# Kernel tuning notes

Hardware: AMD Instinct MI355X
Metric: run time of the kernel (lower is better)

## Reference

```python
import jax, jax.numpy as jnp
import numpy as np

N = 100000
IN_CH = 256
HID = 64
OUT_CH = 40
E1 = 1_600_000
E2 = 3_200_000


def spmm(rows, cols, vals, x, n):
    # out[r] = sum over edges e with rows[e]==r of vals[e] * x[cols[e]]
    return jax.ops.segment_sum(vals[:, None] * x[cols], rows, num_segments=n)


def setup_inputs() -> dict:
    key = jax.random.key(0)
    ks = jax.random.split(key, 12)
    x = jax.random.normal(ks[0], (N, IN_CH), dtype=jnp.float32)
    edge_index = jax.random.randint(ks[1], (2, E1), 0, N, dtype=jnp.int32)
    adj_src = jax.random.randint(ks[2], (E1,), 0, N, dtype=jnp.int32)
    adj_dst = jax.random.randint(ks[3], (E1,), 0, N, dtype=jnp.int32)
    adj_val = jax.random.uniform(ks[4], (E1,), dtype=jnp.float32)
    adj2_src = jax.random.randint(ks[5], (E2,), 0, N, dtype=jnp.int32)
    adj2_dst = jax.random.randint(ks[6], (E2,), 0, N, dtype=jnp.int32)
    adj2_val = jax.random.uniform(ks[7], (E2,), dtype=jnp.float32)
    fc1_w = jax.random.normal(ks[8], (HID, IN_CH), dtype=jnp.float32) * (1.0 / np.sqrt(IN_CH))
    fc_out_w = jax.random.normal(ks[9], (OUT_CH, 3 * HID), dtype=jnp.float32) * (1.0 / np.sqrt(3 * HID))
    fc_out_b = jax.random.normal(ks[10], (OUT_CH,), dtype=jnp.float32) * 0.01
    return {"x": x, "edge_index": edge_index,
            "adj_src": adj_src, "adj_dst": adj_dst, "adj_val": adj_val,
            "adj2_src": adj2_src, "adj2_dst": adj2_dst, "adj2_val": adj2_val,
            "fc1_w": fc1_w, "fc_out_w": fc_out_w, "fc_out_b": fc_out_b}


def reference(x, edge_index, adj_src, adj_dst, adj_val,
              adj2_src, adj2_dst, adj2_val, fc1_w, fc_out_w, fc_out_b):
    # h0 = fc1(x), no bias
    h0 = x @ fc1_w.T                                  # [N, HID]
    # num_layers = 1: one round of 1-hop and 2-hop propagation
    h1 = spmm(adj_src, adj_dst, adj_val, h0, N)       # [N, HID]
    h2 = spmm(adj2_src, adj2_dst, adj2_val, h0, N)    # [N, HID]
    h = jnp.concatenate([h0, h1, h2], axis=1)         # [N, 3*HID]
    # dropout is identity in eval mode
    return h @ fc_out_w.T + fc_out_b                  # [N, OUT_CH]
```

## Files before the change

kernel.cpp:

```cpp
#include <hip/hip_runtime.h>

#define Nn 100000
#define INC 256
#define OC 40
#define GEL 5242880u
#define NB 1563
#define CAP64 3744
#define CHUNK 4096
#define OVFCAP 65536
#define BSTRIDE 264

#define MP_OFF   0
#define G_OFF    131072
#define GCUR_OFF (G_OFF + 20971520)
#define OVFC_OFF (GCUR_OFF + 6256)
#define OVFL_OFF (OVFC_OFF + 8)
#define PAY_OFF  (OVFL_OFF + OVFCAP*12)

typedef __attribute__((ext_vector_type(8))) short bf16x8;
typedef __attribute__((ext_vector_type(4))) float f32x4;

__device__ __forceinline__ unsigned short f2bf(float f) {
    unsigned b = __float_as_uint(f);
    b += 0x7FFFu + ((b >> 16) & 1u);
    return (unsigned short)(b >> 16);
}
__device__ __forceinline__ float bf2f(unsigned short u) {
    return __uint_as_float(((unsigned)u) << 16);
}

__device__ __forceinline__ void fma8(float4& a0, float4& a1, uint4 u, float v) {
    a0.x = fmaf(v, __uint_as_float(u.x << 16), a0.x);
    a0.y = fmaf(v, __uint_as_float(u.x & 0xFFFF0000u), a0.y);
    a0.z = fmaf(v, __uint_as_float(u.y << 16), a0.z);
    a0.w = fmaf(v, __uint_as_float(u.y & 0xFFFF0000u), a0.w);
    a1.x = fmaf(v, __uint_as_float(u.z << 16), a1.x);
    a1.y = fmaf(v, __uint_as_float(u.z & 0xFFFF0000u), a1.y);
    a1.z = fmaf(v, __uint_as_float(u.w << 16), a1.z);
    a1.w = fmaf(v, __uint_as_float(u.w & 0xFFFF0000u), a1.w);
}

__global__ void make_M(const float* __restrict__ fc1_w,
                       const float* __restrict__ fc_out_w,
                       unsigned short* __restrict__ Mb) {
    int j = blockIdx.x;
    int k = threadIdx.x;
    float acc = 0.f;
    if (j < 120) {
        int i = j / 40, o = j - i * 40;
        const float* wrow = fc_out_w + o * 192 + i * 64;
#pragma unroll 8
        for (int t = 0; t < 64; ++t)
            acc = fmaf(wrow[t], fc1_w[t * 256 + k], acc);
    }
    Mb[j * 256 + k] = (j < 120) ? f2bf(acc) : (unsigned short)0;
}

__global__ __launch_bounds__(512, 4) void gemm_mfma(
    const float* __restrict__ x, const unsigned short* __restrict__ Mb,
    const float* __restrict__ bias, float* __restrict__ out,
    unsigned short* __restrict__ g) {
    __shared__ unsigned short mlds[120 * BSTRIDE];
    const int tid = threadIdx.x;
    const int w = tid >> 6;
    const int l = tid & 63;
    const int lane15 = l & 15;
    const int quad = l >> 4;

    for (int i = tid; i < 3840; i += 512) {
        int r = i >> 5;
        int k8 = (i & 31) * 8;
        uint4 v = *(const uint4*)(Mb + r * 256 + k8);
        *(uint4*)(mlds + r * BSTRIDE + k8) = v;
    }
    __syncthreads();

    const int arow = blockIdx.x * 128 + w * 16 + lane15;
    const bool rok = arow < Nn;
    const float* xp = x + (size_t)arow * INC + quad * 8;

    f32x4 acc[8];
#pragma unroll
    for (int c = 0; c < 8; ++c) acc[c] = (f32x4){0.f, 0.f, 0.f, 0.f};

    float4 pa[3], pb_[3];
#pragma unroll
    for (int p = 0; p < 2; ++p) {
        pa[p] = make_float4(0, 0, 0, 0); pb_[p] = make_float4(0, 0, 0, 0);
        if (rok) { pa[p] = *(const float4*)(xp + p * 32); pb_[p] = *(const float4*)(xp + p * 32 + 4); }
    }

#pragma unroll
    for (int kt = 0; kt < 8; ++kt) {
        const int nb = (kt + 2) % 3;
        if (kt + 2 < 8) {
            pa[nb] = make_float4(0, 0, 0, 0); pb_[nb] = make_float4(0, 0, 0, 0);
            if (rok) {
                pa[nb] = *(const float4*)(xp + (kt + 2) * 32);
                pb_[nb] = *(const float4*)(xp + (kt + 2) * 32 + 4);
            }
        }
        const int cu = kt % 3;
        bf16x8 af;
        af[0] = (short)f2bf(pa[cu].x); af[1] = (short)f2bf(pa[cu].y);
        af[2] = (short)f2bf(pa[cu].z); af[3] = (short)f2bf(pa[cu].w);
        af[4] = (short)f2bf(pb_[cu].x); af[5] = (short)f2bf(pb_[cu].y);
        af[6] = (short)f2bf(pb_[cu].z); af[7] = (short)f2bf(pb_[cu].w);
        const unsigned short* bbase = mlds + kt * 32 + quad * 8 + lane15 * BSTRIDE;
#pragma unroll
        for (int ct = 0; ct < 8; ++ct) {
            if (ct * 16 >= 120) break;
            bf16x8 bf = *(const bf16x8*)(bbase + ct * 16 * BSTRIDE);
            acc[ct] = __builtin_amdgcn_mfma_f32_16x16x32_bf16(af, bf, acc[ct], 0, 0, 0);
        }
    }

#pragma unroll
    for (int ct = 0; ct < 8; ++ct) {
        int col = ct * 16 + lane15;
        if (col >= 120) continue;
        int ib = col / 40;
        int cc = col - ib * 40;
        float badd = (ib == 0) ? bias[cc] : 0.f;
#pragma unroll
        for (int reg = 0; reg < 4; ++reg) {
            int gr = blockIdx.x * 128 + w * 16 + quad * 4 + reg;
            if (gr >= Nn) continue;
            float v = acc[ct][reg] + badd;
            if (ib == 0) out[gr * 40 + cc] = v;
            else g[(unsigned)(ib - 1) * GEL + (unsigned)gr * 40u + cc] = f2bf(v);
        }
    }
}

__global__ __launch_bounds__(1024, 8) void partition(
    const int* __restrict__ s1, const int* __restrict__ d1, const float* __restrict__ v1, int E1,
    const int* __restrict__ s2, const int* __restrict__ d2, const float* __restrict__ v2, int E2,
    int* __restrict__ gcur, uint2* __restrict__ payload,
    int* __restrict__ ovf_cnt, unsigned* __restrict__ ovf) {
    __shared__ int cnt[NB];
    __shared__ int loff[NB + 1];
    __shared__ int gbase[NB];
    __shared__ int scanbuf[1024];
    __shared__ uint2 pay[CHUNK];
    __shared__ unsigned short dest16[CHUNK];

    const int t = threadIdx.x;
    const int Etot = E1 + E2;
    const int e0 = blockIdx.x * CHUNK;

    for (int i = t; i < NB; i += 1024) cnt[i] = 0;
    __syncthreads();

    int my_b[4]; int my_rank[4]; unsigned my_p[4]; float my_v[4]; bool my_ok[4];
#pragma unroll
    for (int j = 0; j < 4; ++j) {
        int e = e0 + j * 1024 + t;
        my_ok[j] = (e < Etot);
        if (my_ok[j]) {
            int s, d; float v; unsigned gbit;
            if (e < E1) { s = s1[e]; d = d1[e]; v = v1[e]; gbit = 0u; }
            else { int e2 = e - E1; s = s2[e2]; d = d2[e2]; v = v2[e2]; gbit = 1u; }
            my_b[j] = s >> 6;
            my_p[j] = (unsigned)d | (gbit << 17) | (((unsigned)s & 63u) << 18);
            my_v[j] = v;
            my_rank[j] = atomicAdd(&cnt[my_b[j]], 1);
        }
    }
    __syncthreads();

    int c0 = (2 * t < NB) ? cnt[2 * t] : 0;
    int c1 = (2 * t + 1 < NB) ? cnt[2 * t + 1] : 0;
    scanbuf[t] = c0 + c1;
    __syncthreads();
    for (int off = 1; off < 1024; off <<= 1) {
        int v = (t >= off) ? scanbuf[t - off] : 0;
        __syncthreads();
        scanbuf[t] += v;
        __syncthreads();
    }
    int ex = scanbuf[t] - (c0 + c1);
    if (2 * t < NB)     loff[2 * t] = ex;
    if (2 * t + 1 < NB) loff[2 * t + 1] = ex + c0;
    if (t == 1023)      loff[NB] = scanbuf[1023];
    __syncthreads();

    for (int i = t; i < NB; i += 1024) {
        int cc = cnt[i];
        gbase[i] = cc ? atomicAdd(&gcur[i], cc) : 0;
    }
    __syncthreads();

#pragma unroll
    for (int j = 0; j < 4; ++j) {
        if (my_ok[j]) {
            int lp = loff[my_b[j]] + my_rank[j];
            pay[lp] = make_uint2(my_p[j], __float_as_uint(my_v[j]));
            dest16[lp] = (unsigned short)my_b[j];
        }
    }
    __syncthreads();

    int tot = loff[NB];
    for (int i = t; i < tot; i += 1024) {
        int b = dest16[i];
        int go = gbase[b] + (i - loff[b]);
        if (go < CAP64) payload[(size_t)b * CAP64 + go] = pay[i];
        else {
            int op = atomicAdd(ovf_cnt, 1);
            if (op < OVFCAP) {
                unsigned px = pay[i].x;
                ovf[3 * op] = ((unsigned)b << 6) | ((px >> 18) & 63u);
                ovf[3 * op + 1] = px;
                ovf[3 * op + 2] = pay[i].y;
            }
        }
    }
}

__global__ __launch_bounds__(640, 7) void bucket_gather(
    const int* __restrict__ gcur, const uint2* __restrict__ payload,
    const unsigned short* __restrict__ g, float* __restrict__ out) {
    __shared__ unsigned spay[CAP64];
    __shared__ int cnt[64];
    __shared__ int sb[64];
    __shared__ int rs[65];
    __shared__ float4 red4[64][10];

    const int t = threadIdx.x;
    const int b = blockIdx.x;
    int n = gcur[b];
    n = (n < CAP64) ? n : CAP64;

    if (t < 64) cnt[t] = 0;
    __syncthreads();

    const uint2* pb = payload + (size_t)b * CAP64;

    uint2 pe[6]; int rk[6];
#pragma unroll
    for (int j = 0; j < 6; ++j) {
        int i = t + j * 640;
        if (i < n) {
            uint2 p = pb[i];
            pe[j] = p;
            rk[j] = atomicAdd(&cnt[(p.x >> 18) & 63u], 1);
        }
    }
    __syncthreads();

    if (t < 64) sb[t] = cnt[t];
    __syncthreads();
    for (int off = 1; off < 64; off <<= 1) {
        int v = 0;
        if (t < 64 && t >= off) v = sb[t - off];
        __syncthreads();
        if (t < 64) sb[t] += v;
        __syncthreads();
    }
    if (t < 64) rs[t] = sb[t] - cnt[t];
    if (t == 63) rs[64] = sb[63];
    __syncthreads();

#pragma unroll
    for (int j = 0; j < 6; ++j) {
        int i = t + j * 640;
        if (i < n) {
            uint2 p = pe[j];
            int pos = rs[(p.x >> 18) & 63u] + rk[j];
            unsigned q = (unsigned)(__uint_as_float(p.y) * 16383.f + 0.5f);
            spay[pos] = (p.x & 0x3FFFFu) | (q << 18);
        }
    }
    __syncthreads();

    const int le = t / 10;
    const int sub = t - le * 10;
    const int grp = (sub >= 5) ? 1 : 0;
    const int q8 = (sub - grp * 5) * 8;
    const float VS = 1.0f / 16383.0f;

    float4 a0 = make_float4(0.f, 0.f, 0.f, 0.f);
    float4 a1 = a0, b0 = a0, b1 = a0;
    const int estart = rs[le];
    const int eend = rs[le + 1];
    int e = estart + grp;
    for (; e + 6 < eend; e += 8) {
        unsigned p0 = spay[e], p1 = spay[e + 2], p2 = spay[e + 4], p3 = spay[e + 6];
        uint4 u0 = *(const uint4*)(g + (p0 & 0x3FFFFu) * 40u + q8);
        uint4 u1 = *(const uint4*)(g + (p1 & 0x3FFFFu) * 40u + q8);
        uint4 u2 = *(const uint4*)(g + (p2 & 0x3FFFFu) * 40u + q8);
        uint4 u3 = *(const uint4*)(g + (p3 & 0x3FFFFu) * 40u + q8);
        fma8(a0, a1, u0, (float)(p0 >> 18) * VS);
        fma8(b0, b1, u1, (float)(p1 >> 18) * VS);
        fma8(a0, a1, u2, (float)(p2 >> 18) * VS);
        fma8(b0, b1, u3, (float)(p3 >> 18) * VS);
    }
    for (; e < eend; e += 2) {
        unsigned p = spay[e];
        uint4 u = *(const uint4*)(g + (p & 0x3FFFFu) * 40u + q8);
        fma8(a0, a1, u, (float)(p >> 18) * VS);
    }
    a0.x += b0.x; a0.y += b0.y; a0.z += b0.z; a0.w += b0.w;
    a1.x += b1.x; a1.y += b1.y; a1.z += b1.z; a1.w += b1.w;

    const int c2 = (q8 >> 2);
    __syncthreads();
    if (grp == 1) { red4[le][c2] = a0; red4[le][c2 + 1] = a1; }
    __syncthreads();
    if (grp == 0) {
        float4 r0 = red4[le][c2];
        float4 r1 = red4[le][c2 + 1];
        int gr = b * 64 + le;
        if (gr < Nn && eend > estart) {
            float* po = out + gr * 40 + q8;
            float4 o0 = *(const float4*)po;
            o0.x += a0.x + r0.x; o0.y += a0.y + r0.y;
            o0.z += a0.z + r0.z; o0.w += a0.w + r0.w;
            *(float4*)po = o0;
            float4 o1 = *(const float4*)(po + 4);
            o1.x += a1.x + r1.x; o1.y += a1.y + r1.y;
            o1.z += a1.z + r1.z; o1.w += a1.w + r1.w;
            *(float4*)(po + 4) = o1;
        }
    }
}

__global__ __launch_bounds__(256) void ovf_scatter(
    const int* __restrict__ ovf_cnt, const unsigned* __restrict__ ovf,
    const unsigned short* __restrict__ g, float* __restrict__ out) {
    int n = *ovf_cnt;
    n = (n < OVFCAP) ? n : OVFCAP;
    int total = n * 40;
    for (int i = blockIdx.x * 256 + threadIdx.x; i < total; i += 2048) {
        int idx = i / 40, c = i % 40;
        unsigned s = ovf[3 * idx];
        unsigned p = ovf[3 * idx + 1];
        float v = __uint_as_float(ovf[3 * idx + 2]);
        unsigned rid = p & 0x3FFFFu;
        float gf = bf2f(g[rid * 40u + c]);
        unsafeAtomicAdd(out + s * 40 + c, v * gf);
    }
}

extern "C" void kernel_launch(void* const* d_in, const int* in_sizes, int n_in,
                              void* d_out, int out_size, void* d_ws, size_t ws_size,
                              hipStream_t stream) {
    const float* x        = (const float*)d_in[0];
    const int*   adj_src  = (const int*)d_in[2];
    const int*   adj_dst  = (const int*)d_in[3];
    const float* adj_val  = (const float*)d_in[4];
    const int*   adj2_src = (const int*)d_in[5];
    const int*   adj2_dst = (const int*)d_in[6];
    const float* adj2_val = (const float*)d_in[7];
    const float* fc1_w    = (const float*)d_in[8];
    const float* fc_out_w = (const float*)d_in[9];
    const float* fc_out_b = (const float*)d_in[10];
    float* out = (float*)d_out;

    char* ws = (char*)d_ws;
    unsigned short* Mb      = (unsigned short*)(ws + MP_OFF);
    unsigned short* g       = (unsigned short*)(ws + G_OFF);
    int*            gcur    = (int*)(ws + GCUR_OFF);
    int*            ovf_cnt = (int*)(ws + OVFC_OFF);
    unsigned*       ovf     = (unsigned*)(ws + OVFL_OFF);
    uint2*          payload = (uint2*)(ws + PAY_OFF);

    const int E1 = in_sizes[2];
    const int E2 = in_sizes[5];
    const int Etot = E1 + E2;

    make_M<<<128, 256, 0, stream>>>(fc1_w, fc_out_w, Mb);
    gemm_mfma<<<(Nn + 127) / 128, 512, 0, stream>>>(x, Mb, fc_out_b, out, g);

    hipMemsetAsync(gcur, 0, (OVFC_OFF - GCUR_OFF) + 8, stream);
    partition<<<(Etot + CHUNK - 1) / CHUNK, 1024, 0, stream>>>(
        adj_src, adj_dst, adj_val, E1, adj2_src, adj2_dst, adj2_val, E2,
        gcur, payload, ovf_cnt, ovf);
    bucket_gather<<<NB, 640, 0, stream>>>(gcur, payload, g, out);
    ovf_scatter<<<8, 256, 0, stream>>>(ovf_cnt, ovf, g, out);
}
```

Before: 384.5 us.

## Replace bucketed partition with per-row fixed-capacity edge slots via global atomics

```diff
diff --git a/kernel.cpp b/kernel.cpp
--- a/kernel.cpp
+++ b/kernel.cpp
@@ -4,17 +4,19 @@
 #define INC 256
 #define OC 40
 #define GEL 5242880u
-#define NB 1563
-#define CAP64 3744
-#define CHUNK 4096
+#define CAPR 96
+#define SPITCH 100
+#define NROWB 128
+#define GBLK 782
+#define NROWA (GBLK * NROWB)
 #define OVFCAP 65536
 #define BSTRIDE 264
 
 #define MP_OFF   0
 #define G_OFF    131072
 #define GCUR_OFF (G_OFF + 20971520)
-#define OVFC_OFF (GCUR_OFF + 6256)
-#define OVFL_OFF (OVFC_OFF + 8)
+#define OVFC_OFF (GCUR_OFF + 400384)
+#define OVFL_OFF (OVFC_OFF + 16)
 #define PAY_OFF  (OVFL_OFF + OVFCAP*12)
 
 typedef __attribute__((ext_vector_type(8))) short bf16x8;
@@ -133,160 +135,71 @@
     }
 }
 
-__global__ __launch_bounds__(1024, 8) void partition(
+__global__ __launch_bounds__(256, 8) void partition(
     const int* __restrict__ s1, const int* __restrict__ d1, const float* __restrict__ v1, int E1,
     const int* __restrict__ s2, const int* __restrict__ d2, const float* __restrict__ v2, int E2,
-    int* __restrict__ gcur, uint2* __restrict__ payload,
+    int* __restrict__ gcur, unsigned* __restrict__ payload,
     int* __restrict__ ovf_cnt, unsigned* __restrict__ ovf) {
-    __shared__ int cnt[NB];
-    __shared__ int loff[NB + 1];
-    __shared__ int gbase[NB];
-    __shared__ int scanbuf[1024];
-    __shared__ uint2 pay[CHUNK];
-    __shared__ unsigned short dest16[CHUNK];
-
     const int t = threadIdx.x;
     const int Etot = E1 + E2;
-    const int e0 = blockIdx.x * CHUNK;
-
-    for (int i = t; i < NB; i += 1024) cnt[i] = 0;
-    __syncthreads();
-
-    int my_b[4]; int my_rank[4]; unsigned my_p[4]; float my_v[4]; bool my_ok[4];
+    const int e0 = blockIdx.x * 1024;
 #pragma unroll
     for (int j = 0; j < 4; ++j) {
-        int e = e0 + j * 1024 + t;
-        my_ok[j] = (e < Etot);
-        if (my_ok[j]) {
-            int s, d; float v; unsigned gbit;
-            if (e < E1) { s = s1[e]; d = d1[e]; v = v1[e]; gbit = 0u; }
-            else { int e2 = e - E1; s = s2[e2]; d = d2[e2]; v = v2[e2]; gbit = 1u; }
-            my_b[j] = s >> 6;
-            my_p[j] = (unsigned)d | (gbit << 17) | (((unsigned)s & 63u) << 18);
-            my_v[j] = v;
-            my_rank[j] = atomicAdd(&cnt[my_b[j]], 1);
-        }
-    }
-    __syncthreads();
-
-    int c0 = (2 * t < NB) ? cnt[2 * t] : 0;
-    int c1 = (2 * t + 1 < NB) ? cnt[2 * t + 1] : 0;
-    scanbuf[t] = c0 + c1;
-    __syncthreads();
-    for (int off = 1; off < 1024; off <<= 1) {
-        int v = (t >= off) ? scanbuf[t - off] : 0;
-        __syncthreads();
-        scanbuf[t] += v;
-        __syncthreads();
-    }
-    int ex = scanbuf[t] - (c0 + c1);
-    if (2 * t < NB)     loff[2 * t] = ex;
-    if (2 * t + 1 < NB) loff[2 * t + 1] = ex + c0;
-    if (t == 1023)      loff[NB] = scanbuf[1023];
-    __syncthreads();
-
-    for (int i = t; i < NB; i += 1024) {
-        int cc = cnt[i];
-        gbase[i] = cc ? atomicAdd(&gcur[i], cc) : 0;
-    }
-    __syncthreads();
-
-#pragma unroll
-    for (int j = 0; j < 4; ++j) {
-        if (my_ok[j]) {
-            int lp = loff[my_b[j]] + my_rank[j];
-            pay[lp] = make_uint2(my_p[j], __float_as_uint(my_v[j]));
-            dest16[lp] = (unsigned short)my_b[j];
-        }
-    }
-    __syncthreads();
-
-    int tot = loff[NB];
-    for (int i = t; i < tot; i += 1024) {
-        int b = dest16[i];
-        int go = gbase[b] + (i - loff[b]);
-        if (go < CAP64) payload[(size_t)b * CAP64 + go] = pay[i];
+        int e = e0 + j * 256 + t;
+        if (e >= Etot) continue;
+        int s, d; float v; unsigned ghi;
+        if (e < E1) { s = s1[e]; d = d1[e]; v = v1[e]; ghi = 0u; }
+        else { int e2 = e - E1; s = s2[e2]; d = d2[e2]; v = v2[e2]; ghi = 1u << 17; }
+        unsigned q = (unsigned)(v * 16383.f + 0.5f);
+        unsigned p = (unsigned)d | ghi | (q << 18);
+        int pos = atomicAdd(&gcur[s], 1);
+        if (pos < CAPR) payload[(size_t)s * CAPR + pos] = p;
         else {
             int op = atomicAdd(ovf_cnt, 1);
             if (op < OVFCAP) {
-                unsigned px = pay[i].x;
-                ovf[3 * op] = ((unsigned)b << 6) | ((px >> 18) & 63u);
-                ovf[3 * op + 1] = px;
-                ovf[3 * op + 2] = pay[i].y;
+                ovf[3 * op] = (unsigned)s;
+                ovf[3 * op + 1] = p & 0x3FFFFu;
+                ovf[3 * op + 2] = __float_as_uint(v);
             }
         }
     }
 }
 
 __global__ __launch_bounds__(640, 7) void bucket_gather(
-    const int* __restrict__ gcur, const uint2* __restrict__ payload,
+    const int* __restrict__ gcur, const unsigned* __restrict__ payload,
     const unsigned short* __restrict__ g, float* __restrict__ out) {
-    __shared__ unsigned spay[CAP64];
-    __shared__ int cnt[64];
-    __shared__ int sb[64];
-    __shared__ int rs[65];
-    __shared__ float4 red4[64][10];
+    __shared__ unsigned spay[NROWB * SPITCH];
+    __shared__ int cnt[NROWB];
 
     const int t = threadIdx.x;
     const int b = blockIdx.x;
-    int n = gcur[b];
-    n = (n < CAP64) ? n : CAP64;
-
-    if (t < 64) cnt[t] = 0;
+
+    if (t < NROWB) {
+        int n = gcur[b * NROWB + t];
+        cnt[t] = (n < CAPR) ? n : CAPR;
+    }
+
+    const unsigned* pbase = payload + (size_t)b * (NROWB * CAPR);
+    for (int i = t; i < NROWB * CAPR / 4; i += 640) {
+        int row = i / (CAPR / 4);
+        int c4 = (i - row * (CAPR / 4)) * 4;
+        uint4 v = *(const uint4*)(pbase + row * CAPR + c4);
+        *(uint4*)(&spay[row * SPITCH + c4]) = v;
+    }
     __syncthreads();
 
-    const uint2* pb = payload + (size_t)b * CAP64;
-
-    uint2 pe[6]; int rk[6];
-#pragma unroll
-    for (int j = 0; j < 6; ++j) {
-        int i = t + j * 640;
-        if (i < n) {
-            uint2 p = pb[i];
-            pe[j] = p;
-            rk[j] = atomicAdd(&cnt[(p.x >> 18) & 63u], 1);
-        }
-    }
-    __syncthreads();
-
-    if (t < 64) sb[t] = cnt[t];
-    __syncthreads();
-    for (int off = 1; off < 64; off <<= 1) {
-        int v = 0;
-        if (t < 64 && t >= off) v = sb[t - off];
-        __syncthreads();
-        if (t < 64) sb[t] += v;
-        __syncthreads();
-    }
-    if (t < 64) rs[t] = sb[t] - cnt[t];
-    if (t == 63) rs[64] = sb[63];
-    __syncthreads();
-
-#pragma unroll
-    for (int j = 0; j < 6; ++j) {
-        int i = t + j * 640;
-        if (i < n) {
-            uint2 p = pe[j];
-            int pos = rs[(p.x >> 18) & 63u] + rk[j];
-            unsigned q = (unsigned)(__uint_as_float(p.y) * 16383.f + 0.5f);
-            spay[pos] = (p.x & 0x3FFFFu) | (q << 18);
-        }
-    }
-    __syncthreads();
-
-    const int le = t / 10;
-    const int sub = t - le * 10;
-    const int grp = (sub >= 5) ? 1 : 0;
-    const int q8 = (sub - grp * 5) * 8;
+    const int le = t / 5;
+    const int q8 = (t - le * 5) * 8;
+    const int base = le * SPITCH;
+    const int n = cnt[le];
     const float VS = 1.0f / 16383.0f;
 
     float4 a0 = make_float4(0.f, 0.f, 0.f, 0.f);
     float4 a1 = a0, b0 = a0, b1 = a0;
-    const int estart = rs[le];
-    const int eend = rs[le + 1];
-    int e = estart + grp;
-    for (; e + 6 < eend; e += 8) {
-        unsigned p0 = spay[e], p1 = spay[e + 2], p2 = spay[e + 4], p3 = spay[e + 6];
+    int e = 0;
+    for (; e + 3 < n; e += 4) {
+        unsigned p0 = spay[base + e], p1 = spay[base + e + 1];
+        unsigned p2 = spay[base + e + 2], p3 = spay[base + e + 3];
         uint4 u0 = *(const uint4*)(g + (p0 & 0x3FFFFu) * 40u + q8);
         uint4 u1 = *(const uint4*)(g + (p1 & 0x3FFFFu) * 40u + q8);
         uint4 u2 = *(const uint4*)(g + (p2 & 0x3FFFFu) * 40u + q8);
@@ -296,33 +209,23 @@
         fma8(a0, a1, u2, (float)(p2 >> 18) * VS);
         fma8(b0, b1, u3, (float)(p3 >> 18) * VS);
     }
-    for (; e < eend; e += 2) {
-        unsigned p = spay[e];
+    for (; e < n; ++e) {
+        unsigned p = spay[base + e];
         uint4 u = *(const uint4*)(g + (p & 0x3FFFFu) * 40u + q8);
         fma8(a0, a1, u, (float)(p >> 18) * VS);
     }
     a0.x += b0.x; a0.y += b0.y; a0.z += b0.z; a0.w += b0.w;
     a1.x += b1.x; a1.y += b1.y; a1.z += b1.z; a1.w += b1.w;
 
-    const int c2 = (q8 >> 2);
-    __syncthreads();
-    if (grp == 1) { red4[le][c2] = a0; red4[le][c2 + 1] = a1; }
-    __syncthreads();
-    if (grp == 0) {
-        float4 r0 = red4[le][c2];
-        float4 r1 = red4[le][c2 + 1];
-        int gr = b * 64 + le;
-        if (gr < Nn && eend > estart) {
-            float* po = out + gr * 40 + q8;
-            float4 o0 = *(const float4*)po;
-            o0.x += a0.x + r0.x; o0.y += a0.y + r0.y;
-            o0.z += a0.z + r0.z; o0.w += a0.w + r0.w;
-            *(float4*)po = o0;
-            float4 o1 = *(const float4*)(po + 4);
-            o1.x += a1.x + r1.x; o1.y += a1.y + r1.y;
-            o1.z += a1.z + r1.z; o1.w += a1.w + r1.w;
-            *(float4*)(po + 4) = o1;
-        }
+    const int gr = b * NROWB + le;
+    if (gr < Nn && n > 0) {
+        float* po = out + gr * 40 + q8;
+        float4 o0 = *(const float4*)po;
+        o0.x += a0.x; o0.y += a0.y; o0.z += a0.z; o0.w += a0.w;
+        *(float4*)po = o0;
+        float4 o1 = *(const float4*)(po + 4);
+        o1.x += a1.x; o1.y += a1.y; o1.z += a1.z; o1.w += a1.w;
+        *(float4*)(po + 4) = o1;
     }
 }
 
@@ -335,9 +238,8 @@
     for (int i = blockIdx.x * 256 + threadIdx.x; i < total; i += 2048) {
         int idx = i / 40, c = i % 40;
         unsigned s = ovf[3 * idx];
-        unsigned p = ovf[3 * idx + 1];
+        unsigned rid = ovf[3 * idx + 1];
         float v = __uint_as_float(ovf[3 * idx + 2]);
-        unsigned rid = p & 0x3FFFFu;
         float gf = bf2f(g[rid * 40u + c]);
         unsafeAtomicAdd(out + s * 40 + c, v * gf);
     }
@@ -364,7 +266,7 @@
     int*            gcur    = (int*)(ws + GCUR_OFF);
     int*            ovf_cnt = (int*)(ws + OVFC_OFF);
     unsigned*       ovf     = (unsigned*)(ws + OVFL_OFF);
-    uint2*          payload = (uint2*)(ws + PAY_OFF);
+    unsigned*       payload = (unsigned*)(ws + PAY_OFF);
 
     const int E1 = in_sizes[2];
     const int E2 = in_sizes[5];
@@ -373,10 +275,10 @@
     make_M<<<128, 256, 0, stream>>>(fc1_w, fc_out_w, Mb);
     gemm_mfma<<<(Nn + 127) / 128, 512, 0, stream>>>(x, Mb, fc_out_b, out, g);
 
-    hipMemsetAsync(gcur, 0, (OVFC_OFF - GCUR_OFF) + 8, stream);
-    partition<<<(Etot + CHUNK - 1) / CHUNK, 1024, 0, stream>>>(
+    hipMemsetAsync(gcur, 0, (OVFL_OFF - GCUR_OFF), stream);
+    partition<<<(Etot + 1023) / 1024, 256, 0, stream>>>(
         adj_src, adj_dst, adj_val, E1, adj2_src, adj2_dst, adj2_val, E2,
         gcur, payload, ovf_cnt, ovf);
-    bucket_gather<<<NB, 640, 0, stream>>>(gcur, payload, g, out);
+    bucket_gather<<<GBLK, 640, 0, stream>>>(gcur, payload, g, out);
     ovf_scatter<<<8, 256, 0, stream>>>(ovf_cnt, ovf, g, out);
 }
```

Result: slower. 597.4 us (+55.4%).

## Replace single-pass 1563-bucket edge partition with two-level 98-superbucket radix partition

Applied to the files above, without the earlier changes.

```diff
diff --git a/kernel.cpp b/kernel.cpp
--- a/kernel.cpp
+++ b/kernel.cpp
@@ -2,20 +2,24 @@
 
 #define Nn 100000
 #define INC 256
-#define OC 40
 #define GEL 5242880u
-#define NB 1563
-#define CAP64 3744
+#define NSB 98
+#define SCAP 51456
+#define NCH2 13
+#define SEGW 288
+#define CREG 4608
+#define SREG 59904
 #define CHUNK 4096
-#define OVFCAP 65536
+#define OVFCAP 32768
 #define BSTRIDE 264
 
 #define MP_OFF   0
-#define G_OFF    131072
-#define GCUR_OFF (G_OFF + 20971520)
-#define OVFC_OFF (GCUR_OFF + 6256)
-#define OVFL_OFF (OVFC_OFF + 8)
-#define PAY_OFF  (OVFL_OFF + OVFCAP*12)
+#define G_OFF    65536
+#define SCUR_OFF 21037056
+#define OVFC_OFF 21043456
+#define OVFL_OFF 21043472
+#define SCNT_OFF 21436688
+#define PAY_OFF  21477648
 
 typedef __attribute__((ext_vector_type(8))) short bf16x8;
 typedef __attribute__((ext_vector_type(4))) float f32x4;
@@ -133,23 +137,22 @@
     }
 }
 
-__global__ __launch_bounds__(1024, 8) void partition(
+__global__ __launch_bounds__(1024, 8) void partition1(
     const int* __restrict__ s1, const int* __restrict__ d1, const float* __restrict__ v1, int E1,
     const int* __restrict__ s2, const int* __restrict__ d2, const float* __restrict__ v2, int E2,
-    int* __restrict__ gcur, uint2* __restrict__ payload,
+    int* __restrict__ scur, uint2* __restrict__ sp,
     int* __restrict__ ovf_cnt, unsigned* __restrict__ ovf) {
-    __shared__ int cnt[NB];
-    __shared__ int loff[NB + 1];
-    __shared__ int gbase[NB];
-    __shared__ int scanbuf[1024];
+    __shared__ int cnt[NSB];
+    __shared__ int loff[NSB + 1];
+    __shared__ int gbase[NSB];
     __shared__ uint2 pay[CHUNK];
-    __shared__ unsigned short dest16[CHUNK];
+    __shared__ unsigned char dest8[CHUNK];
 
     const int t = threadIdx.x;
     const int Etot = E1 + E2;
     const int e0 = blockIdx.x * CHUNK;
 
-    for (int i = t; i < NB; i += 1024) cnt[i] = 0;
+    for (int i = t; i < NSB; i += 1024) cnt[i] = 0;
     __syncthreads();
 
     int my_b[4]; int my_rank[4]; unsigned my_p[4]; float my_v[4]; bool my_ok[4];
@@ -161,33 +164,24 @@
             int s, d; float v; unsigned gbit;
             if (e < E1) { s = s1[e]; d = d1[e]; v = v1[e]; gbit = 0u; }
             else { int e2 = e - E1; s = s2[e2]; d = d2[e2]; v = v2[e2]; gbit = 1u; }
-            my_b[j] = s >> 6;
-            my_p[j] = (unsigned)d | (gbit << 17) | (((unsigned)s & 63u) << 18);
+            my_b[j] = s >> 10;
+            my_p[j] = (unsigned)d | (gbit << 17) | (((unsigned)s & 1023u) << 18);
             my_v[j] = v;
             my_rank[j] = atomicAdd(&cnt[my_b[j]], 1);
         }
     }
     __syncthreads();
 
-    int c0 = (2 * t < NB) ? cnt[2 * t] : 0;
-    int c1 = (2 * t + 1 < NB) ? cnt[2 * t + 1] : 0;
-    scanbuf[t] = c0 + c1;
-    __syncthreads();
-    for (int off = 1; off < 1024; off <<= 1) {
-        int v = (t >= off) ? scanbuf[t - off] : 0;
-        __syncthreads();
-        scanbuf[t] += v;
-        __syncthreads();
-    }
-    int ex = scanbuf[t] - (c0 + c1);
-    if (2 * t < NB)     loff[2 * t] = ex;
-    if (2 * t + 1 < NB) loff[2 * t + 1] = ex + c0;
-    if (t == 1023)      loff[NB] = scanbuf[1023];
-    __syncthreads();
-
-    for (int i = t; i < NB; i += 1024) {
-        int cc = cnt[i];
-        gbase[i] = cc ? atomicAdd(&gcur[i], cc) : 0;
+    if (t == 0) {
+        int run = 0;
+        for (int i = 0; i < NSB; ++i) { loff[i] = run; run += cnt[i]; }
+        loff[NSB] = run;
+    }
+    __syncthreads();
+
+    if (t < NSB) {
+        int cc = cnt[t];
+        gbase[t] = cc ? atomicAdd(&scur[t * 16], cc) : 0;
     }
     __syncthreads();
 
@@ -196,21 +190,21 @@
         if (my_ok[j]) {
             int lp = loff[my_b[j]] + my_rank[j];
             pay[lp] = make_uint2(my_p[j], __float_as_uint(my_v[j]));
-            dest16[lp] = (unsigned short)my_b[j];
-        }
-    }
-    __syncthreads();
-
-    int tot = loff[NB];
+            dest8[lp] = (unsigned char)my_b[j];
+        }
+    }
+    __syncthreads();
+
+    int tot = loff[NSB];
     for (int i = t; i < tot; i += 1024) {
-        int b = dest16[i];
-        int go = gbase[b] + (i - loff[b]);
-        if (go < CAP64) payload[(size_t)b * CAP64 + go] = pay[i];
+        int bk = dest8[i];
+        int go = gbase[bk] + (i - loff[bk]);
+        if (go < SCAP) sp[(size_t)bk * SREG + go] = pay[i];
         else {
             int op = atomicAdd(ovf_cnt, 1);
             if (op < OVFCAP) {
                 unsigned px = pay[i].x;
-                ovf[3 * op] = ((unsigned)b << 6) | ((px >> 18) & 63u);
+                ovf[3 * op] = (unsigned)(bk << 10) | ((px >> 18) & 1023u);
                 ovf[3 * op + 1] = px;
                 ovf[3 * op + 2] = pay[i].y;
             }
@@ -218,33 +212,127 @@
     }
 }
 
+__global__ __launch_bounds__(1024, 2) void partition2(
+    const int* __restrict__ scur, uint2* __restrict__ pay,
+    unsigned short* __restrict__ scnt,
+    int* __restrict__ ovf_cnt, unsigned* __restrict__ ovf) {
+    __shared__ int cntb[16][16];
+    __shared__ int woff[16][16];
+
+    const int t = threadIdx.x;
+    const int w = t >> 6;
+    const int sbk = blockIdx.x;
+    int m = scur[sbk * 16];
+    if (m > SCAP) m = SCAP;
+    uint2* base = pay + (size_t)sbk * SREG;
+
+    uint2 pc[4]; int okc[4];
+    {
+        int lo = (NCH2 - 1) * CHUNK;
+        int sz = m - lo; if (sz > CHUNK) sz = CHUNK;
+#pragma unroll
+        for (int k = 0; k < 4; ++k) {
+            int i = t + k * 1024;
+            okc[k] = (i < sz);
+            pc[k] = okc[k] ? base[lo + i] : make_uint2(0u, 0u);
+        }
+    }
+    for (int j = NCH2 - 1; j >= 0; --j) {
+        uint2 pn[4]; int okn[4];
+#pragma unroll
+        for (int k = 0; k < 4; ++k) { pn[k] = make_uint2(0u, 0u); okn[k] = 0; }
+        if (j > 0) {
+            int lo2 = (j - 1) * CHUNK;
+            int sz2 = m - lo2; if (sz2 > CHUNK) sz2 = CHUNK;
+#pragma unroll
+            for (int k = 0; k < 4; ++k) {
+                int i = t + k * 1024;
+                okn[k] = (i < sz2);
+                if (okn[k]) pn[k] = base[lo2 + i];
+            }
+        }
+        if (t < 256) cntb[t >> 4][t & 15] = 0;
+        __syncthreads();
+        int rk[4], fn[4];
+#pragma unroll
+        for (int k = 0; k < 4; ++k) {
+            fn[k] = 0; rk[k] = 0;
+            if (okc[k]) {
+                fn[k] = (pc[k].x >> 24) & 15;
+                rk[k] = atomicAdd(&cntb[w][fn[k]], 1);
+            }
+        }
+        __syncthreads();
+        if (t < 16) {
+            int run = 0;
+#pragma unroll
+            for (int ww = 0; ww < 16; ++ww) { woff[ww][t] = run; run += cntb[ww][t]; }
+            scnt[(sbk * NCH2 + j) * 16 + t] = (unsigned short)(run < SEGW ? run : SEGW);
+        }
+        __syncthreads();
+        uint2* cbase = base + (size_t)j * CREG;
+#pragma unroll
+        for (int k = 0; k < 4; ++k) {
+            if (okc[k]) {
+                int pos = woff[w][fn[k]] + rk[k];
+                if (pos < SEGW) cbase[fn[k] * SEGW + pos] = pc[k];
+                else {
+                    int op = atomicAdd(ovf_cnt, 1);
+                    if (op < OVFCAP) {
+                        unsigned px = pc[k].x;
+                        ovf[3 * op] = (unsigned)(sbk << 10) | ((px >> 18) & 1023u);
+                        ovf[3 * op + 1] = px;
+                        ovf[3 * op + 2] = pc[k].y;
+                    }
+                }
+            }
+        }
+#pragma unroll
+        for (int k = 0; k < 4; ++k) { pc[k] = pn[k]; okc[k] = okn[k]; }
+    }
+}
+
 __global__ __launch_bounds__(640, 7) void bucket_gather(
-    const int* __restrict__ gcur, const uint2* __restrict__ payload,
+    const unsigned short* __restrict__ scnt, const uint2* __restrict__ pay,
     const unsigned short* __restrict__ g, float* __restrict__ out) {
-    __shared__ unsigned spay[CAP64];
+    __shared__ unsigned spay[NCH2 * SEGW];
     __shared__ int cnt[64];
     __shared__ int sb[64];
     __shared__ int rs[65];
+    __shared__ int sps[NCH2 + 1];
     __shared__ float4 red4[64][10];
 
     const int t = threadIdx.x;
     const int b = blockIdx.x;
-    int n = gcur[b];
-    n = (n < CAP64) ? n : CAP64;
+    const int sbk = b >> 4;
+    const int f = b & 15;
 
     if (t < 64) cnt[t] = 0;
-    __syncthreads();
-
-    const uint2* pb = payload + (size_t)b * CAP64;
+    if (t < NCH2) sps[t + 1] = (int)scnt[(sbk * NCH2 + t) * 16 + f];
+    __syncthreads();
+    if (t == 0) {
+        sps[0] = 0;
+        int run = 0;
+#pragma unroll
+        for (int j = 0; j < NCH2; ++j) { run += sps[j + 1]; sps[j + 1] = run; }
+    }
+    __syncthreads();
+    const int n = sps[NCH2];
+
+    const uint2* pb = pay + (size_t)sbk * SREG + f * SEGW;
 
     uint2 pe[6]; int rk[6];
 #pragma unroll
-    for (int j = 0; j < 6; ++j) {
-        int i = t + j * 640;
+    for (int jj = 0; jj < 6; ++jj) {
+        int i = t + jj * 640;
         if (i < n) {
-            uint2 p = pb[i];
-            pe[j] = p;
-            rk[j] = atomicAdd(&cnt[(p.x >> 18) & 63u], 1);
+            int j = 0;
+#pragma unroll
+            for (int q = 1; q < NCH2; ++q) j += (i >= sps[q]);
+            int off = i - sps[j];
+            uint2 p = pb[(size_t)j * CREG + off];
+            pe[jj] = p;
+            rk[jj] = atomicAdd(&cnt[(p.x >> 18) & 63u], 1);
         }
     }
     __syncthreads();
@@ -263,11 +351,11 @@
     __syncthreads();
 
 #pragma unroll
-    for (int j = 0; j < 6; ++j) {
-        int i = t + j * 640;
+    for (int jj = 0; jj < 6; ++jj) {
+        int i = t + jj * 640;
         if (i < n) {
-            uint2 p = pe[j];
-            int pos = rs[(p.x >> 18) & 63u] + rk[j];
+            uint2 p = pe[jj];
+            int pos = rs[(p.x >> 18) & 63u] + rk[jj];
             unsigned q = (unsigned)(__uint_as_float(p.y) * 16383.f + 0.5f);
             spay[pos] = (p.x & 0x3FFFFu) | (q << 18);
         }
@@ -361,9 +449,10 @@
     char* ws = (char*)d_ws;
     unsigned short* Mb      = (unsigned short*)(ws + MP_OFF);
     unsigned short* g       = (unsigned short*)(ws + G_OFF);
-    int*            gcur    = (int*)(ws + GCUR_OFF);
+    int*            scur    = (int*)(ws + SCUR_OFF);
     int*            ovf_cnt = (int*)(ws + OVFC_OFF);
     unsigned*       ovf     = (unsigned*)(ws + OVFL_OFF);
+    unsigned short* scnt    = (unsigned short*)(ws + SCNT_OFF);
     uint2*          payload = (uint2*)(ws + PAY_OFF);
 
     const int E1 = in_sizes[2];
@@ -373,10 +462,11 @@
     make_M<<<128, 256, 0, stream>>>(fc1_w, fc_out_w, Mb);
     gemm_mfma<<<(Nn + 127) / 128, 512, 0, stream>>>(x, Mb, fc_out_b, out, g);
 
-    hipMemsetAsync(gcur, 0, (OVFC_OFF - GCUR_OFF) + 8, stream);
-    partition<<<(Etot + CHUNK - 1) / CHUNK, 1024, 0, stream>>>(
+    hipMemsetAsync(scur, 0, (OVFC_OFF - SCUR_OFF) + 16, stream);
+    partition1<<<(Etot + CHUNK - 1) / CHUNK, 1024, 0, stream>>>(
         adj_src, adj_dst, adj_val, E1, adj2_src, adj2_dst, adj2_val, E2,
-        gcur, payload, ovf_cnt, ovf);
-    bucket_gather<<<NB, 640, 0, stream>>>(gcur, payload, g, out);
+        scur, payload, ovf_cnt, ovf);
+    partition2<<<NSB, 1024, 0, stream>>>(scur, payload, scnt, ovf_cnt, ovf);
+    bucket_gather<<<NSB * 16, 640, 0, stream>>>(scnt, payload, g, out);
     ovf_scatter<<<8, 256, 0, stream>>>(ovf_cnt, ovf, g, out);
 }
```

New measurement: 539.4 us. 1.4x slower.
